# Kernel tuning notes

Measured on AMD Instinct MI355X. Metric: run time of the kernel, lower is better.

Reference implementation:

```python
import jax, jax.numpy as jnp
import numpy as np

COST_CLASS, COST_BBOX, COST_GIOU = 1.0, 5.0, 2.0


def box_cxcywh_to_xyxy(b):
    cx, cy, w, h = jnp.split(b, 4, axis=-1)
    return jnp.concatenate([cx - 0.5 * w, cy - 0.5 * h, cx + 0.5 * w, cy + 0.5 * h], axis=-1)


def generalized_box_iou(a, b):
    # a: [N,4] xyxy, b: [M,4] xyxy -> [N,M]
    area_a = (a[:, 2] - a[:, 0]) * (a[:, 3] - a[:, 1])
    area_b = (b[:, 2] - b[:, 0]) * (b[:, 3] - b[:, 1])
    lt = jnp.maximum(a[:, None, :2], b[None, :, :2])
    rb = jnp.minimum(a[:, None, 2:], b[None, :, 2:])
    wh = jnp.clip(rb - lt, 0.0)
    inter = wh[..., 0] * wh[..., 1]
    union = area_a[:, None] + area_b[None, :] - inter
    iou = inter / union
    lt2 = jnp.minimum(a[:, None, :2], b[None, :, :2])
    rb2 = jnp.maximum(a[:, None, 2:], b[None, :, 2:])
    wh2 = jnp.clip(rb2 - lt2, 0.0)
    encl = wh2[..., 0] * wh2[..., 1]
    return iou - (encl - union) / encl


@jax.jit
def _cost_matrix(pred_logits, pred_boxes, tgt_labels, tgt_boxes):
    bs, Q, _ = pred_logits.shape
    out_prob = jax.nn.softmax(pred_logits.reshape(bs * Q, -1), axis=-1)   # [bs*Q, C]
    out_bbox = pred_boxes.reshape(bs * Q, 4)                              # [bs*Q, 4]
    tgt_ids = tgt_labels.reshape(-1)                                      # [bs*T]
    tgt_bb = tgt_boxes.reshape(-1, 4)                                     # [bs*T, 4]
    cost_class = 1.0 - out_prob[:, tgt_ids]                               # [bs*Q, bs*T]
    cost_bbox = jnp.sum(jnp.abs(out_bbox[:, None, :] - tgt_bb[None, :, :]), axis=-1)  # L1 cdist
    cost_giou = 1.0 - generalized_box_iou(box_cxcywh_to_xyxy(out_bbox), box_cxcywh_to_xyxy(tgt_bb))
    C = COST_BBOX * cost_bbox + COST_CLASS * cost_class + COST_GIOU * cost_giou
    return C.reshape(bs, Q, -1)                                           # [bs, Q, bs*T]


def _lsa(cost):
    # Hungarian (shortest augmenting path / Jonker-Volgenant), cost: [n, m], n <= m.
    # Returns, for each row i, the assigned column (globally optimal assignment).
    n, m = cost.shape
    INF = 1e18
    u = np.zeros(n + 1)
    v = np.zeros(m + 1)
    p = np.zeros(m + 1, dtype=np.int64)    # p[j] = row matched to column j (1-indexed, 0 = free)
    way = np.zeros(m + 1, dtype=np.int64)
    for i in range(1, n + 1):
        p[0] = i
        j0 = 0
        minv = np.full(m + 1, INF)
        used = np.zeros(m + 1, dtype=bool)
        while True:
            used[j0] = True
            i0 = p[j0]
            cur = cost[i0 - 1] - u[i0] - v[1:]
            mask = ~used[1:]
            upd = mask & (cur < minv[1:])
            minv[1:] = np.where(upd, cur, minv[1:])
            way[1:] = np.where(upd, j0, way[1:])
            cand = np.where(mask, minv[1:], INF)
            j1 = int(np.argmin(cand)) + 1
            delta = cand[j1 - 1]
            u[p[used]] += delta
            v[used] -= delta
            minv[1:] = np.where(mask, minv[1:] - delta, minv[1:])
            j0 = j1
            if p[j0] == 0:
                break
        while j0:
            j1 = way[j0]
            p[j0] = p[j1]
            j0 = j1
    rows = np.zeros(n, dtype=np.int64)
    for j in range(1, m + 1):
        if p[j] > 0:
            rows[p[j] - 1] = j - 1
    return rows


def setup_inputs() -> dict:
    key = jax.random.key(0)
    k1, k2, k3, k4 = jax.random.split(key, 4)
    bs, Q, C, T = 32, 900, 91, 30
    return {
        'pred_logits': jax.random.normal(k1, (bs, Q, C), dtype=jnp.float32),
        'pred_boxes': jax.random.uniform(k2, (bs, Q, 4), dtype=jnp.float32),
        'tgt_labels': jax.random.randint(k3, (bs, T), 0, C),
        'tgt_boxes': jax.random.uniform(k4, (bs, T, 4), dtype=jnp.float32),
    }


def reference(pred_logits, pred_boxes, tgt_labels, tgt_boxes):
    C3 = _cost_matrix(pred_logits, pred_boxes, tgt_labels, tgt_boxes)  # [bs, Q, bs*T]
    bs, Q, _ = C3.shape
    T = tgt_labels.shape[1]
    C_np = np.asarray(jax.device_get(C3), dtype=np.float64)
    pred_idx = np.zeros((bs, T), dtype=np.int64)
    tgt_idx = np.zeros((bs, T), dtype=np.int64)
    for i in range(bs):
        c = C_np[i, :, i * T:(i + 1) * T]        # per-image block [Q, T] (== split-by-sizes)
        preds = _lsa(c.T)                        # for each target, matched prediction
        order = np.argsort(preds, kind='stable') # scipy returns row indices sorted ascending
        pred_idx[i] = preds[order]
        tgt_idx[i] = np.arange(T, dtype=np.int64)[order]
    return C3, jnp.asarray(pred_idx), jnp.asarray(tgt_idx)
```

## Files before the change

### kernel.cpp

```cpp
#include <hip/hip_runtime.h>
#include <math.h>

#define BS 32
#define NQ 900
#define NC 91
#define NT 30
#define NJ (BS*NT)
#define C3_SZ ((size_t)BS*NQ*NJ)
#define NROWS (BS*NQ)

#define LT 960
#define LWAVES (LT/64)
#define NCOSTBLK 224
#define MAXROWS 132

__device__ __forceinline__ float fast_rcp(float x) { return __builtin_amdgcn_rcpf(x); }

struct SharedLSA {
    float  cst[NT * NQ];
    double u[NT + 1];
    int    p[NQ + 1];
    int    way[NQ + 1];
    double red_v[LWAVES];
    int    red_i[LWAVES];
    int    rows[NT];
    float  rminv[NT];
    int    rminc[NT];
    int    aflag[NT + 1];
};
struct SharedCost {
    float  prob[MAXROWS][NC];
    float4 pbx[MAXROWS];
};

__device__ __forceinline__ float cost_elem(
    float pcx, float pcy, float pw, float ph,
    float px0, float py0, float px1, float py1, float area_a,
    float pr,
    float tcx, float tcy, float tw, float th,
    float tx0, float ty0, float tx1, float ty1, float area_b)
{
    float cost_bbox = fabsf(pcx - tcx) + fabsf(pcy - tcy) + fabsf(pw - tw) + fabsf(ph - th);
    float ix0 = fmaxf(px0, tx0), iy0 = fmaxf(py0, ty0);
    float ix1 = fminf(px1, tx1), iy1 = fminf(py1, ty1);
    float inter = fmaxf(ix1 - ix0, 0.f) * fmaxf(iy1 - iy0, 0.f);
    float uni = area_a + area_b - inter;
    float iou = inter * fast_rcp(uni);
    float ex0 = fminf(px0, tx0), ey0 = fminf(py0, ty0);
    float ex1 = fmaxf(px1, tx1), ey1 = fmaxf(py1, ty1);
    float encl = fmaxf(ex1 - ex0, 0.f) * fmaxf(ey1 - ey0, 0.f);
    float giou = iou - (encl - uni) * fast_rcp(encl);
    return 5.0f * cost_bbox - pr - 2.0f * giou + 3.0f;
}

__device__ __forceinline__ void softmax_prob_row(const float* __restrict__ lrow, int lane,
                                                 float* __restrict__ prob)
{
    float a = (lane < NC)      ? lrow[lane]      : -1e30f;
    float c = (lane + 64 < NC) ? lrow[lane + 64] : -1e30f;
    float m = fmaxf(a, c);
    for (int off = 32; off; off >>= 1) m = fmaxf(m, __shfl_xor(m, off));
    float ea = (lane < NC)      ? __expf(a - m) : 0.f;
    float ec = (lane + 64 < NC) ? __expf(c - m) : 0.f;
    float s = ea + ec;
    for (int off = 32; off; off >>= 1) s += __shfl_xor(s, off);
    float rs = fast_rcp(s);
    if (lane < NC)      prob[lane]      = ea * rs;
    if (lane + 64 < NC) prob[lane + 64] = ec * rs;
}

__global__ __launch_bounds__(LT) void fused_kernel(
    const float* __restrict__ logits,
    const float* __restrict__ pboxes,
    const int*   __restrict__ tlabels,
    const float* __restrict__ tboxes,
    float* __restrict__ out,
    float* __restrict__ outp,
    float* __restrict__ outt,
    int*   __restrict__ flags)
{
    __shared__ union { SharedLSA l; SharedCost c; } sm;
    const int t = threadIdx.x;
    const int wv = t >> 6;
    const int lane = t & 63;

    if (blockIdx.x >= BS) {
        const int cb = blockIdx.x - BS;
        const int r0 = (int)(((long long)cb * NROWS) / NCOSTBLK);
        const int r1 = (int)(((long long)(cb + 1) * NROWS) / NCOSTBLK);
        const int nrows = r1 - r0;

        for (int rr = wv; rr < nrows; rr += LWAVES)
            softmax_prob_row(logits + (size_t)(r0 + rr) * NC, lane, sm.c.prob[rr]);
        for (int rr = t; rr < nrows; rr += LT)
            sm.c.pbx[rr] = ((const float4*)pboxes)[r0 + rr];
        __syncthreads();

        for (int e = t; e < nrows * NT; e += LT) {
            int rr  = e / NT;
            int r   = e - rr * NT;
            int row = r0 + rr;
            int bb  = row / NQ;
            int col = bb * NT + r;
            float pr = sm.c.prob[rr][tlabels[col]];
            float4 pb = sm.c.pbx[rr];
            float pcx = pb.x, pcy = pb.y, pw = pb.z, ph = pb.w;
            float px0 = pcx - 0.5f*pw, py0 = pcy - 0.5f*ph;
            float px1 = pcx + 0.5f*pw, py1 = pcy + 0.5f*ph;
            float area_a = pw * ph;
            float4 tb2 = ((const float4*)tboxes)[col];
            float tcx = tb2.x, tcy = tb2.y, tw = tb2.z, th = tb2.w;
            float tx0 = tcx - 0.5f*tw, ty0 = tcy - 0.5f*th;
            float tx1 = tcx + 0.5f*tw, ty1 = tcy + 0.5f*th;
            float area_b = tw * th;
            out[(size_t)row * NJ + col] =
                cost_elem(pcx, pcy, pw, ph, px0, py0, px1, py1, area_a,
                          pr, tcx, tcy, tw, th, tx0, ty0, tx1, ty1, area_b);
        }
        __syncthreads();
        if (t == 0) {
            __threadfence();
            int b_lo = r0 / NQ, b_hi = (r1 - 1) / NQ;
            for (int bb = b_lo; bb <= b_hi; ++bb)
                atomicAdd(&flags[bb], 1);
        }

        const int   lbl = tlabels[t];
        const float4 tb = ((const float4*)tboxes)[t];
        const float tcx = tb.x, tcy = tb.y, tw = tb.z, th = tb.w;
        const float tx0 = tcx - 0.5f*tw, ty0 = tcy - 0.5f*th;
        const float tx1 = tcx + 0.5f*tw, ty1 = tcy + 0.5f*th;
        const float area_b = tw * th;
        const unsigned drow0 = (unsigned)((t / NT) * NQ);

        float* op = out + (size_t)r0 * NJ + t;
        #pragma unroll 2
        for (int rr = 0; rr < nrows; ++rr) {
            const int row = r0 + rr;
            float pr = sm.c.prob[rr][lbl];
            float4 pb = sm.c.pbx[rr];
            float pcx = pb.x, pcy = pb.y, pw = pb.z, ph = pb.w;
            float px0 = pcx - 0.5f*pw, py0 = pcy - 0.5f*ph;
            float px1 = pcx + 0.5f*pw, py1 = pcy + 0.5f*ph;
            float area_a = pw * ph;
            float v = cost_elem(pcx, pcy, pw, ph, px0, py0, px1, py1, area_a,
                                pr, tcx, tcy, tw, th, tx0, ty0, tx1, ty1, area_b);
            if ((unsigned)row - drow0 >= (unsigned)NQ)
                __builtin_nontemporal_store(v, op);
            op += NJ;
        }
    } else {
        const int b = blockIdx.x;

        for (int j = t; j <= NQ; j += LT) { sm.l.p[j] = 0; sm.l.way[j] = 0; }

        int exp_cnt = 0;
        for (int cb = 0; cb < NCOSTBLK; ++cb) {
            int a0 = (int)(((long long)cb * NROWS) / NCOSTBLK);
            int a1 = (int)(((long long)(cb + 1) * NROWS) / NCOSTBLK);
            if (a0 < (b + 1) * NQ && a1 > b * NQ) ++exp_cnt;
        }
        if (t == 0) {
            while (__hip_atomic_load(&flags[b], __ATOMIC_ACQUIRE,
                                     __HIP_MEMORY_SCOPE_AGENT) < exp_cnt)
                __builtin_amdgcn_s_sleep(2);
        }
        __syncthreads();
        __threadfence();

        const float* src = out + (size_t)b * NQ * NJ + (size_t)b * NT;
        for (int e = t; e < NT * NQ; e += LT) {
            int q = e / NT;
            int r = e - q * NT;
            sm.l.cst[r * NQ + q] = src[(size_t)q * NJ + r];
        }
        __syncthreads();

        for (int r = wv; r < NT; r += LWAVES) {
            float bv = 1e30f; int bi = 1 << 20;
            for (int j = lane; j < NQ; j += 64) {
                float v = sm.l.cst[r * NQ + j];
                if (v < bv) { bv = v; bi = j; }
            }
            for (int off = 32; off; off >>= 1) {
                float ov = __shfl_xor(bv, off);
                int   oi = __shfl_xor(bi, off);
                if (ov < bv || (ov == bv && oi < bi)) { bv = ov; bi = oi; }
            }
            if (lane == 0) { sm.l.rminv[r] = bv; sm.l.rminc[r] = bi + 1; }
        }
        __syncthreads();

        if (wv == 0) {
            int r = lane;
            int myc = (r < NT) ? sm.l.rminc[r] : -1;
            bool win = (r < NT);
            for (int j = 0; j < NT; ++j) {
                int cj = __shfl(myc, j);
                if (j < r && cj == myc) win = false;
            }
            if (r < NT) {
                sm.l.u[r + 1] = (double)sm.l.rminv[r];
                sm.l.aflag[r + 1] = win ? 1 : 0;
                if (win) sm.l.p[myc] = r + 1;
            }
        }
        double v_t = 0.0;
        __syncthreads();

        for (int i = 1; i <= NT; ++i) {
            if (sm.l.aflag[i]) continue;
            double minv_t = 1e18;
            bool used_t = (t == 0);
            int p_t = (t == 0) ? i : ((t <= NQ) ? sm.l.p[t] : 0);
            int i0 = i, j0 = 0, j1f = 0;
            for (;;) {
                double u_i0 = sm.l.u[i0];
                double cand; int ci;
                if (t >= 1 && t <= NQ && !used_t) {
                    double cur = ((double)sm.l.cst[(i0 - 1) * NQ + (t - 1)] - u_i0) - v_t;
                    if (cur < minv_t) { minv_t = cur; sm.l.way[t] = j0; }
                    cand = minv_t; ci = t;
                } else { cand = 1e18; ci = 1 << 20; }
                for (int off = 32; off; off >>= 1) {
                    double ov = __shfl_xor(cand, off);
                    int    oi = __shfl_xor(ci, off);
                    if (ov < cand || (ov == cand && oi < ci)) { cand = ov; ci = oi; }
                }
                if (lane == 0) { sm.l.red_v[wv] = cand; sm.l.red_i[wv] = ci; }
                __syncthreads();
                double rv; int ri;
                if (lane < LWAVES) { rv = sm.l.red_v[lane]; ri = sm.l.red_i[lane]; }
                else               { rv = 1e18;             ri = 1 << 20; }
                for (int off = 8; off; off >>= 1) {
                    double ov = __shfl_xor(rv, off);
                    int    oi = __shfl_xor(ri, off);
                    if (ov < rv || (ov == rv && oi < ri)) { rv = ov; ri = oi; }
                }
                double delta = __shfl(rv, 0);
                int    j1    = __shfl(ri, 0);
                if (used_t) { v_t -= delta; sm.l.u[p_t] += delta; }
                else if (t >= 1 && t <= NQ) minv_t -= delta;
                if (t == j1) { used_t = true; p_t = sm.l.p[j1]; }
                int pj1 = sm.l.p[j1];
                __syncthreads();
                if (pj1 == 0) { j1f = j1; break; }
                i0 = pj1; j0 = j1;
            }
            if (t == 0) {
                int j0w = j1f;
                while (j0w) {
                    int jp = sm.l.way[j0w];
                    sm.l.p[j0w] = (jp == 0) ? i : sm.l.p[jp];
                    j0w = jp;
                }
            }
            __syncthreads();
        }
        if (t >= 1 && t <= NQ && sm.l.p[t] > 0) sm.l.rows[sm.l.p[t] - 1] = t - 1;
        __syncthreads();

        if (wv == 0) {
            int k = lane;
            int key = (k < NT) ? sm.l.rows[k] : 0x7fffffff;
            int rank = 0;
            for (int j = 0; j < NT; ++j) {
                int kj = __shfl(key, j);
                if (kj < key) ++rank;
            }
            if (k < NT) {
                outp[b * NT + rank] = (float)key;
                outt[b * NT + rank] = (float)k;
            }
        }
    }
}

extern "C" void kernel_launch(void* const* d_in, const int* in_sizes, int n_in,
                              void* d_out, int out_size, void* d_ws, size_t ws_size,
                              hipStream_t stream) {
    const float* logits  = (const float*)d_in[0];
    const float* pboxes  = (const float*)d_in[1];
    const int*   tlabels = (const int*)d_in[2];
    const float* tboxes  = (const float*)d_in[3];
    float* out  = (float*)d_out;
    int* flags  = (int*)d_ws;

    hipMemsetAsync(flags, 0, BS * sizeof(int), stream);
    fused_kernel<<<BS + NCOSTBLK, LT, 0, stream>>>(
        logits, pboxes, tlabels, tboxes,
        out, out + C3_SZ, out + C3_SZ + (size_t)BS * NT, flags);
}
```

Before: 200.9 us.

## Merge LSA blocks into cost blocks so every block computes costs first

```diff
diff --git a/kernel.cpp b/kernel.cpp
--- a/kernel.cpp
+++ b/kernel.cpp
@@ -11,8 +11,8 @@
 
 #define LT 960
 #define LWAVES (LT/64)
-#define NCOSTBLK 224
-#define MAXROWS 132
+#define NBLK 256
+#define MAXROWS 113
 
 __device__ __forceinline__ float fast_rcp(float x) { return __builtin_amdgcn_rcpf(x); }
 
@@ -84,59 +84,28 @@
     const int wv = t >> 6;
     const int lane = t & 63;
 
-    if (blockIdx.x >= BS) {
-        const int cb = blockIdx.x - BS;
-        const int r0 = (int)(((long long)cb * NROWS) / NCOSTBLK);
-        const int r1 = (int)(((long long)(cb + 1) * NROWS) / NCOSTBLK);
-        const int nrows = r1 - r0;
-
-        for (int rr = wv; rr < nrows; rr += LWAVES)
-            softmax_prob_row(logits + (size_t)(r0 + rr) * NC, lane, sm.c.prob[rr]);
-        for (int rr = t; rr < nrows; rr += LT)
-            sm.c.pbx[rr] = ((const float4*)pboxes)[r0 + rr];
-        __syncthreads();
-
-        for (int e = t; e < nrows * NT; e += LT) {
-            int rr  = e / NT;
-            int r   = e - rr * NT;
-            int row = r0 + rr;
-            int bb  = row / NQ;
-            int col = bb * NT + r;
-            float pr = sm.c.prob[rr][tlabels[col]];
-            float4 pb = sm.c.pbx[rr];
-            float pcx = pb.x, pcy = pb.y, pw = pb.z, ph = pb.w;
-            float px0 = pcx - 0.5f*pw, py0 = pcy - 0.5f*ph;
-            float px1 = pcx + 0.5f*pw, py1 = pcy + 0.5f*ph;
-            float area_a = pw * ph;
-            float4 tb2 = ((const float4*)tboxes)[col];
-            float tcx = tb2.x, tcy = tb2.y, tw = tb2.z, th = tb2.w;
-            float tx0 = tcx - 0.5f*tw, ty0 = tcy - 0.5f*th;
-            float tx1 = tcx + 0.5f*tw, ty1 = tcy + 0.5f*th;
-            float area_b = tw * th;
-            out[(size_t)row * NJ + col] =
-                cost_elem(pcx, pcy, pw, ph, px0, py0, px1, py1, area_a,
-                          pr, tcx, tcy, tw, th, tx0, ty0, tx1, ty1, area_b);
-        }
-        __syncthreads();
-        if (t == 0) {
-            __threadfence();
-            int b_lo = r0 / NQ, b_hi = (r1 - 1) / NQ;
-            for (int bb = b_lo; bb <= b_hi; ++bb)
-                atomicAdd(&flags[bb], 1);
-        }
-
+    const int cb = blockIdx.x;
+    const int r0 = (int)(((long long)cb * NROWS) / NBLK);
+    const int r1 = (int)(((long long)(cb + 1) * NROWS) / NBLK);
+    const int nrows = r1 - r0;
+
+    for (int rr = wv; rr < nrows; rr += LWAVES)
+        softmax_prob_row(logits + (size_t)(r0 + rr) * NC, lane, sm.c.prob[rr]);
+    for (int rr = t; rr < nrows; rr += LT)
+        sm.c.pbx[rr] = ((const float4*)pboxes)[r0 + rr];
+
+    {
         const int   lbl = tlabels[t];
         const float4 tb = ((const float4*)tboxes)[t];
         const float tcx = tb.x, tcy = tb.y, tw = tb.z, th = tb.w;
         const float tx0 = tcx - 0.5f*tw, ty0 = tcy - 0.5f*th;
         const float tx1 = tcx + 0.5f*tw, ty1 = tcy + 0.5f*th;
         const float area_b = tw * th;
-        const unsigned drow0 = (unsigned)((t / NT) * NQ);
+        __syncthreads();
 
         float* op = out + (size_t)r0 * NJ + t;
         #pragma unroll 2
         for (int rr = 0; rr < nrows; ++rr) {
-            const int row = r0 + rr;
             float pr = sm.c.prob[rr][lbl];
             float4 pb = sm.c.pbx[rr];
             float pcx = pb.x, pcy = pb.y, pw = pb.z, ph = pb.w;
@@ -145,133 +114,142 @@
             float area_a = pw * ph;
             float v = cost_elem(pcx, pcy, pw, ph, px0, py0, px1, py1, area_a,
                                 pr, tcx, tcy, tw, th, tx0, ty0, tx1, ty1, area_b);
-            if ((unsigned)row - drow0 >= (unsigned)NQ)
-                __builtin_nontemporal_store(v, op);
+            __builtin_nontemporal_store(v, op);
             op += NJ;
         }
-    } else {
-        const int b = blockIdx.x;
-
-        for (int j = t; j <= NQ; j += LT) { sm.l.p[j] = 0; sm.l.way[j] = 0; }
-
-        int exp_cnt = 0;
-        for (int cb = 0; cb < NCOSTBLK; ++cb) {
-            int a0 = (int)(((long long)cb * NROWS) / NCOSTBLK);
-            int a1 = (int)(((long long)(cb + 1) * NROWS) / NCOSTBLK);
-            if (a0 < (b + 1) * NQ && a1 > b * NQ) ++exp_cnt;
+    }
+    __syncthreads();
+    if (t == 0) {
+        __threadfence();
+        int b_lo = r0 / NQ, b_hi = (r1 - 1) / NQ;
+        for (int bb = b_lo; bb <= b_hi; ++bb)
+            atomicAdd(&flags[bb], 1);
+    }
+    if (blockIdx.x >= BS) return;
+
+    const int b = blockIdx.x;
+
+    for (int j = t; j <= NQ; j += LT) { sm.l.p[j] = 0; sm.l.way[j] = 0; }
+
+    int exp_cnt = 0;
+    for (int c2 = 0; c2 < NBLK; ++c2) {
+        int a0 = (int)(((long long)c2 * NROWS) / NBLK);
+        int a1 = (int)(((long long)(c2 + 1) * NROWS) / NBLK);
+        if (a0 < (b + 1) * NQ && a1 > b * NQ) ++exp_cnt;
+    }
+    if (t == 0) {
+        int guard = 1 << 22;
+        while (__hip_atomic_load(&flags[b], __ATOMIC_ACQUIRE,
+                                 __HIP_MEMORY_SCOPE_AGENT) < exp_cnt && --guard)
+            __builtin_amdgcn_s_sleep(2);
+    }
+    __syncthreads();
+    __threadfence();
+
+    const float* src = out + (size_t)b * NQ * NJ + (size_t)b * NT;
+    for (int e = t; e < NT * NQ; e += LT) {
+        int q = e / NT;
+        int r = e - q * NT;
+        sm.l.cst[r * NQ + q] = src[(size_t)q * NJ + r];
+    }
+    __syncthreads();
+
+    for (int r = wv; r < NT; r += LWAVES) {
+        float bv = 1e30f; int bi = 1 << 20;
+        for (int j = lane; j < NQ; j += 64) {
+            float v = sm.l.cst[r * NQ + j];
+            if (v < bv) { bv = v; bi = j; }
+        }
+        for (int off = 32; off; off >>= 1) {
+            float ov = __shfl_xor(bv, off);
+            int   oi = __shfl_xor(bi, off);
+            if (ov < bv || (ov == bv && oi < bi)) { bv = ov; bi = oi; }
+        }
+        if (lane == 0) { sm.l.rminv[r] = bv; sm.l.rminc[r] = bi + 1; }
+    }
+    __syncthreads();
+
+    if (wv == 0) {
+        int r = lane;
+        int myc = (r < NT) ? sm.l.rminc[r] : -1;
+        bool win = (r < NT) && (myc >= 1 && myc <= NQ);
+        for (int j = 0; j < NT; ++j) {
+            int cj = __shfl(myc, j);
+            if (j < r && cj == myc) win = false;
+        }
+        if (r < NT) {
+            sm.l.u[r + 1] = (double)sm.l.rminv[r];
+            sm.l.aflag[r + 1] = win ? 1 : 0;
+            if (win) sm.l.p[myc] = r + 1;
+        }
+    }
+    double v_t = 0.0;
+    __syncthreads();
+
+    for (int i = 1; i <= NT; ++i) {
+        if (sm.l.aflag[i]) continue;
+        double minv_t = 1e18;
+        bool used_t = (t == 0);
+        int p_t = (t == 0) ? i : ((t <= NQ) ? sm.l.p[t] : 0);
+        int i0 = i, j0 = 0, j1f = 0;
+        for (;;) {
+            double u_i0 = sm.l.u[i0];
+            double cand; int ci;
+            if (t >= 1 && t <= NQ && !used_t) {
+                double cur = ((double)sm.l.cst[(i0 - 1) * NQ + (t - 1)] - u_i0) - v_t;
+                if (cur < minv_t) { minv_t = cur; sm.l.way[t] = j0; }
+                cand = minv_t; ci = t;
+            } else { cand = 1e18; ci = 1 << 20; }
+            for (int off = 32; off; off >>= 1) {
+                double ov = __shfl_xor(cand, off);
+                int    oi = __shfl_xor(ci, off);
+                if (ov < cand || (ov == cand && oi < ci)) { cand = ov; ci = oi; }
+            }
+            if (lane == 0) { sm.l.red_v[wv] = cand; sm.l.red_i[wv] = ci; }
+            __syncthreads();
+            double rv; int ri;
+            if (lane < LWAVES) { rv = sm.l.red_v[lane]; ri = sm.l.red_i[lane]; }
+            else               { rv = 1e18;             ri = 1 << 20; }
+            for (int off = 8; off; off >>= 1) {
+                double ov = __shfl_xor(rv, off);
+                int    oi = __shfl_xor(ri, off);
+                if (ov < rv || (ov == rv && oi < ri)) { rv = ov; ri = oi; }
+            }
+            double delta = __shfl(rv, 0);
+            int    j1    = __shfl(ri, 0);
+            if (used_t) { v_t -= delta; sm.l.u[p_t] += delta; }
+            else if (t >= 1 && t <= NQ) minv_t -= delta;
+            if (t == j1) { used_t = true; p_t = sm.l.p[j1]; }
+            int pj1 = (j1 >= 0 && j1 <= NQ) ? sm.l.p[j1] : 0;
+            __syncthreads();
+            if (pj1 == 0) { j1f = j1; break; }
+            i0 = pj1; j0 = j1;
         }
         if (t == 0) {
-            while (__hip_atomic_load(&flags[b], __ATOMIC_ACQUIRE,
-                                     __HIP_MEMORY_SCOPE_AGENT) < exp_cnt)
-                __builtin_amdgcn_s_sleep(2);
+            int j0w = (j1f >= 0 && j1f <= NQ) ? j1f : 0;
+            int guard = NQ + 1;
+            while (j0w && guard--) {
+                int jp = sm.l.way[j0w];
+                sm.l.p[j0w] = (jp == 0) ? i : sm.l.p[jp];
+                j0w = jp;
+            }
         }
         __syncthreads();
-        __threadfence();
-
-        const float* src = out + (size_t)b * NQ * NJ + (size_t)b * NT;
-        for (int e = t; e < NT * NQ; e += LT) {
-            int q = e / NT;
-            int r = e - q * NT;
-            sm.l.cst[r * NQ + q] = src[(size_t)q * NJ + r];
-        }
-        __syncthreads();
-
-        for (int r = wv; r < NT; r += LWAVES) {
-            float bv = 1e30f; int bi = 1 << 20;
-            for (int j = lane; j < NQ; j += 64) {
-                float v = sm.l.cst[r * NQ + j];
-                if (v < bv) { bv = v; bi = j; }
-            }
-            for (int off = 32; off; off >>= 1) {
-                float ov = __shfl_xor(bv, off);
-                int   oi = __shfl_xor(bi, off);
-                if (ov < bv || (ov == bv && oi < bi)) { bv = ov; bi = oi; }
-            }
-            if (lane == 0) { sm.l.rminv[r] = bv; sm.l.rminc[r] = bi + 1; }
-        }
-        __syncthreads();
-
-        if (wv == 0) {
-            int r = lane;
-            int myc = (r < NT) ? sm.l.rminc[r] : -1;
-            bool win = (r < NT);
-            for (int j = 0; j < NT; ++j) {
-                int cj = __shfl(myc, j);
-                if (j < r && cj == myc) win = false;
-            }
-            if (r < NT) {
-                sm.l.u[r + 1] = (double)sm.l.rminv[r];
-                sm.l.aflag[r + 1] = win ? 1 : 0;
-                if (win) sm.l.p[myc] = r + 1;
-            }
-        }
-        double v_t = 0.0;
-        __syncthreads();
-
-        for (int i = 1; i <= NT; ++i) {
-            if (sm.l.aflag[i]) continue;
-            double minv_t = 1e18;
-            bool used_t = (t == 0);
-            int p_t = (t == 0) ? i : ((t <= NQ) ? sm.l.p[t] : 0);
-            int i0 = i, j0 = 0, j1f = 0;
-            for (;;) {
-                double u_i0 = sm.l.u[i0];
-                double cand; int ci;
-                if (t >= 1 && t <= NQ && !used_t) {
-                    double cur = ((double)sm.l.cst[(i0 - 1) * NQ + (t - 1)] - u_i0) - v_t;
-                    if (cur < minv_t) { minv_t = cur; sm.l.way[t] = j0; }
-                    cand = minv_t; ci = t;
-                } else { cand = 1e18; ci = 1 << 20; }
-                for (int off = 32; off; off >>= 1) {
-                    double ov = __shfl_xor(cand, off);
-                    int    oi = __shfl_xor(ci, off);
-                    if (ov < cand || (ov == cand && oi < ci)) { cand = ov; ci = oi; }
-                }
-                if (lane == 0) { sm.l.red_v[wv] = cand; sm.l.red_i[wv] = ci; }
-                __syncthreads();
-                double rv; int ri;
-                if (lane < LWAVES) { rv = sm.l.red_v[lane]; ri = sm.l.red_i[lane]; }
-                else               { rv = 1e18;             ri = 1 << 20; }
-                for (int off = 8; off; off >>= 1) {
-                    double ov = __shfl_xor(rv, off);
-                    int    oi = __shfl_xor(ri, off);
-                    if (ov < rv || (ov == rv && oi < ri)) { rv = ov; ri = oi; }
-                }
-                double delta = __shfl(rv, 0);
-                int    j1    = __shfl(ri, 0);
-                if (used_t) { v_t -= delta; sm.l.u[p_t] += delta; }
-                else if (t >= 1 && t <= NQ) minv_t -= delta;
-                if (t == j1) { used_t = true; p_t = sm.l.p[j1]; }
-                int pj1 = sm.l.p[j1];
-                __syncthreads();
-                if (pj1 == 0) { j1f = j1; break; }
-                i0 = pj1; j0 = j1;
-            }
-            if (t == 0) {
-                int j0w = j1f;
-                while (j0w) {
-                    int jp = sm.l.way[j0w];
-                    sm.l.p[j0w] = (jp == 0) ? i : sm.l.p[jp];
-                    j0w = jp;
-                }
-            }
-            __syncthreads();
-        }
-        if (t >= 1 && t <= NQ && sm.l.p[t] > 0) sm.l.rows[sm.l.p[t] - 1] = t - 1;
-        __syncthreads();
-
-        if (wv == 0) {
-            int k = lane;
-            int key = (k < NT) ? sm.l.rows[k] : 0x7fffffff;
-            int rank = 0;
-            for (int j = 0; j < NT; ++j) {
-                int kj = __shfl(key, j);
-                if (kj < key) ++rank;
-            }
-            if (k < NT) {
-                outp[b * NT + rank] = (float)key;
-                outt[b * NT + rank] = (float)k;
-            }
+    }
+    if (t >= 1 && t <= NQ && sm.l.p[t] > 0) sm.l.rows[sm.l.p[t] - 1] = t - 1;
+    __syncthreads();
+
+    if (wv == 0) {
+        int k = lane;
+        int key = (k < NT) ? sm.l.rows[k] : 0x7fffffff;
+        int rank = 0;
+        for (int j = 0; j < NT; ++j) {
+            int kj = __shfl(key, j);
+            if (kj < key) ++rank;
+        }
+        if (k < NT) {
+            outp[b * NT + rank] = (float)key;
+            outt[b * NT + rank] = (float)k;
         }
     }
 }
@@ -287,7 +265,7 @@
     int* flags  = (int*)d_ws;
 
     hipMemsetAsync(flags, 0, BS * sizeof(int), stream);
-    fused_kernel<<<BS + NCOSTBLK, LT, 0, stream>>>(
+    fused_kernel<<<NBLK, LT, 0, stream>>>(
         logits, pboxes, tlabels, tboxes,
         out, out + C3_SZ, out + C3_SZ + (size_t)BS * NT, flags);
 }
```

New measurement: 199.4 us. No clear change (-0.7%).
